# Performance work log

Hardware: AMD Instinct MI355X
Metric: run time of the kernel (lower is better)

The kernel has to match this reference:

```python
import jax, jax.numpy as jnp
import numpy as np

N = 50000   # nodes
E = 800000  # edges (avg degree 16)
F = 128     # n_input
H = 8       # n_heads
C = 16      # n_hidden (per-head out channels)
D = H * C   # 128


def setup_inputs() -> dict:
    key = jax.random.key(0)
    ks = jax.random.split(key, 12)
    s = lambda k, shape: (jax.random.normal(k, shape, dtype=jnp.float32) * 0.05)
    return {
        'x': jax.random.normal(ks[0], (N, F), dtype=jnp.float32),
        'edge_index': jax.random.randint(ks[1], (2, E), 0, N, dtype=jnp.int32),
        # GATv2Conv params (PyG defaults: share_weights=False, bias=True, neg_slope=0.2, self-loops)
        'W_l': s(ks[2], (F, D)),
        'b_l': jnp.zeros((D,), jnp.float32),
        'W_r': s(ks[3], (F, D)),
        'b_r': jnp.zeros((D,), jnp.float32),
        'att': s(ks[4], (H, C)),
        'conv_bias': jnp.zeros((D,), jnp.float32),
        # BatchNorm1d affine params
        'bn_gamma': jnp.ones((D,), jnp.float32),
        'bn_beta': jnp.zeros((D,), jnp.float32),
        # encoder output Linear
        'lin_W': s(ks[5], (D, D)),
        'lin_b': jnp.zeros((D,), jnp.float32),
        # EdgeDecoder scalars a, b (init 1.0)
        'a_edge': jnp.ones((1,), jnp.float32),
        'b_edge': jnp.ones((1,), jnp.float32),
        # LinearDecoder
        'dec2_W': s(ks[6], (D, F)),
        'dec2_b': jnp.zeros((F,), jnp.float32),
    }


def reference(x, edge_index, W_l, b_l, W_r, b_r, att, conv_bias,
              bn_gamma, bn_beta, lin_W, lin_b, a_edge, b_edge, dec2_W, dec2_b):
    n = x.shape[0]
    # GATv2Conv adds self-loops by default
    loop = jnp.arange(n, dtype=edge_index.dtype)
    src = jnp.concatenate([edge_index[0], loop])  # source j (messages come from)
    dst = jnp.concatenate([edge_index[1], loop])  # target i (softmax segments)
    xl = (x @ W_l + b_l).reshape(n, H, C)  # source transform
    xr = (x @ W_r + b_r).reshape(n, H, C)  # target transform
    # attention logits: a^T LeakyReLU(xl_j + xr_i), per head
    e = jax.nn.leaky_relu(xl[src] + xr[dst], negative_slope=0.2)  # [Et,H,C]
    logits = jnp.einsum('ehc,hc->eh', e, att)                     # [Et,H]
    # segment softmax over incoming edges of each target node
    m = jax.ops.segment_max(logits, dst, num_segments=n)
    ex = jnp.exp(logits - m[dst])
    denom = jax.ops.segment_sum(ex, dst, num_segments=n)
    alpha = ex / (denom[dst] + 1e-16)                             # [Et,H]
    # scatter-sum weighted source features, concat heads, add bias
    out = jax.ops.segment_sum(alpha[:, :, None] * xl[src], dst, num_segments=n)
    Hfeat = jax.nn.relu(out.reshape(n, D) + conv_bias)
    # BatchNorm1d, training-mode batch statistics (biased var), eps=1e-5
    mean = Hfeat.mean(axis=0)
    var = Hfeat.var(axis=0)
    Hn = (Hfeat - mean) / jnp.sqrt(var + 1e-5) * bn_gamma + bn_beta
    z = Hn @ lin_W + lin_b                                        # [N,D]
    # EdgeDecoder: gather + squared-diff + reduce over original edges
    dist = jnp.sum((z[edge_index[0]] - z[edge_index[1]]) ** 2, axis=1)  # [E]
    dist = jax.nn.relu(a_edge) * dist + b_edge
    value1 = jax.nn.sigmoid(-dist)                                # [E]
    # LinearDecoder
    value2 = z @ dec2_W + dec2_b                                  # [N,F]
    return (z, value1, value2)
```

## Files before the change

### kernel.cpp

```cpp
#include <hip/hip_runtime.h>

#define DD 128
#define HH 8
#define NBCOPY 32

typedef float f32x4 __attribute__((ext_vector_type(4)));
typedef short s16x8 __attribute__((ext_vector_type(8)));

__device__ __forceinline__ ushort f2b(float f) {
  unsigned u = __float_as_uint(f);
  unsigned r = u + 0x7fffu + ((u >> 16) & 1u);
  return (ushort)(r >> 16);
}
__device__ __forceinline__ float b2f(ushort b) {
  return __uint_as_float(((unsigned)b) << 16);
}
__device__ __forceinline__ void atomAddF(float* p, float v) {
#if defined(__HIP_DEVICE_COMPILE__)
  unsafeAtomicAdd(p, v);
#else
  atomicAdd(p, v);
#endif
}
__device__ __forceinline__ float lrelu(float v) { return fmaxf(v, 0.2f * v); }

__device__ __forceinline__ float sumC(const float* __restrict__ b8, int idx) {
  float s = 0.f;
#pragma unroll
  for (int c = 0; c < NBCOPY; c++) s += b8[(c << 8) + idx];
  return s;
}

__device__ __forceinline__ void packW_idx(int i, int& k, int& n) {
  int j = i & 7, l = (i >> 3) & 63, tile = i >> 9;
  int q = tile >> 3, c = tile & 7;
  k = q * 32 + ((l >> 4) << 3) + j;
  n = c * 16 + (l & 15);
}

__global__ __launch_bounds__(256) void k_prep(const float* __restrict__ x,
    ushort* __restrict__ xb, int total4, const float* __restrict__ Wl,
    const float* __restrict__ Wr, ushort* __restrict__ WlP,
    ushort* __restrict__ WrP, const int* __restrict__ ei,
    int* __restrict__ deg, int E, int convB, int packB) {
  int b = blockIdx.x;
  if (b < convB) {
    int i = b * 256 + threadIdx.x;
    if (i < total4) {
      float4 v = ((const float4*)x)[i];
      ushort4 o;
      o.x = f2b(v.x); o.y = f2b(v.y); o.z = f2b(v.z); o.w = f2b(v.w);
      ((ushort4*)xb)[i] = o;
    }
  } else if (b < convB + packB) {
    int t = (b - convB) * 256 + threadIdx.x;
    int side = t >> 14;
    int i = t & 16383;
    int k, n;
    packW_idx(i, k, n);
    if (side) WrP[i] = f2b(Wr[k * DD + n]);
    else      WlP[i] = f2b(Wl[k * DD + n]);
  } else {
    int e = (b - convB - packB) * 256 + threadIdx.x;
    if (e < E) atomicAdd(&deg[ei[E + e]], 1);
  }
}

__global__ __launch_bounds__(256) void k_part(const int* __restrict__ deg,
    int* __restrict__ rowstart, int* __restrict__ bsum, int N) {
  __shared__ int sc[256];
  int t = threadIdx.x;
  int i = blockIdx.x * 256 + t;
  int v = (i < N) ? deg[i] : 0;
  sc[t] = v;
  __syncthreads();
  for (int off = 1; off < 256; off <<= 1) {
    int u = (t >= off) ? sc[t - off] : 0;
    __syncthreads();
    sc[t] += u;
    __syncthreads();
  }
  if (i < N) rowstart[i] = sc[t] - v;
  if (t == 255) bsum[blockIdx.x] = sc[255];
}

__global__ __launch_bounds__(1024) void k_mid(const int* __restrict__ bsum,
    int* __restrict__ boff, int* __restrict__ rowstartN, int B) {
  __shared__ int sc[1024];
  int t = threadIdx.x;
  int v = (t < B) ? bsum[t] : 0;
  sc[t] = v;
  __syncthreads();
  for (int off = 1; off < 1024; off <<= 1) {
    int u = (t >= off) ? sc[t - off] : 0;
    __syncthreads();
    sc[t] += u;
    __syncthreads();
  }
  if (t < B) boff[t] = sc[t] - v;
  if (t == 1023) *rowstartN = sc[1023];
}

__global__ __launch_bounds__(256) void k_apply(int* __restrict__ rowstart,
    int* __restrict__ cursor, const int* __restrict__ boff, int N) {
  int i = blockIdx.x * 256 + threadIdx.x;
  if (i < N) {
    int r = rowstart[i] + boff[blockIdx.x];
    rowstart[i] = r;
    cursor[i] = r;
  }
}

__global__ __launch_bounds__(256) void k_fill(const int* __restrict__ ei,
    int* __restrict__ cursor, int* __restrict__ csr_src, int E) {
  int e = blockIdx.x * 256 + threadIdx.x;
  if (e < E) {
    int d = ei[E + e];
    int pos = atomicAdd(&cursor[d], 1);
    csr_src[pos] = ei[e];
  }
}

__global__ __launch_bounds__(256) void k_mm_lr(const ushort* __restrict__ xb,
    const ushort* __restrict__ WlP, const ushort* __restrict__ WrP,
    const float* __restrict__ bl, const float* __restrict__ br,
    ushort* __restrict__ xlb, ushort* __restrict__ xrb, int N) {
  __shared__ ushort sW[2][16384];
  {
    const uint4* a = (const uint4*)WlP;
    const uint4* b = (const uint4*)WrP;
    uint4* da = (uint4*)sW[0];
    uint4* db = (uint4*)sW[1];
    for (int i = threadIdx.x; i < 2048; i += 256) { da[i] = a[i]; db[i] = b[i]; }
  }
  __syncthreads();
  int lane = threadIdx.x & 63;
  int wv = threadIdx.x >> 6;
  int rbase = blockIdx.x * 64 + wv * 16;
  int arow = rbase + (lane & 15);
  if (arow >= N) arow = 0;
  const ushort* ap = xb + (size_t)arow * DD + ((lane >> 4) << 3);
  s16x8 afr[4];
#pragma unroll
  for (int q = 0; q < 4; q++) afr[q] = *(const s16x8*)(ap + q * 32);
  f32x4 accL[8] = {}, accR[8] = {};
#pragma unroll
  for (int q = 0; q < 4; q++) {
#pragma unroll
    for (int c = 0; c < 8; c++) {
      s16x8 bL = *(const s16x8*)(sW[0] + ((q * 8 + c) * 64 + lane) * 8);
      accL[c] = __builtin_amdgcn_mfma_f32_16x16x32_bf16(afr[q], bL, accL[c], 0, 0, 0);
      s16x8 bR = *(const s16x8*)(sW[1] + ((q * 8 + c) * 64 + lane) * 8);
      accR[c] = __builtin_amdgcn_mfma_f32_16x16x32_bf16(afr[q], bR, accR[c], 0, 0, 0);
    }
  }
  int r0 = rbase + ((lane >> 4) << 2);
  int colb = lane & 15;
#pragma unroll
  for (int c = 0; c < 8; c++) {
    int col = c * 16 + colb;
    float vbl = bl[col], vbr = br[col];
#pragma unroll
    for (int r = 0; r < 4; r++) {
      int row = r0 + r;
      if (row < N) {
        xlb[(size_t)row * DD + col] = f2b(accL[c][r] + vbl);
        xrb[(size_t)row * DD + col] = f2b(accR[c][r] + vbr);
      }
    }
  }
}

__global__ __launch_bounds__(256) void k_mm_z(const ushort* __restrict__ hfb,
    const ushort* __restrict__ W1P, const ushort* __restrict__ W2P,
    const float* __restrict__ b1p, const float* __restrict__ b2pp,
    float* __restrict__ z, ushort* __restrict__ zb, float* __restrict__ v2,
    int N) {
  __shared__ ushort sW[2][16384];
  {
    const uint4* a = (const uint4*)W1P;
    const uint4* b = (const uint4*)W2P;
    uint4* da = (uint4*)sW[0];
    uint4* db = (uint4*)sW[1];
    for (int i = threadIdx.x; i < 2048; i += 256) { da[i] = a[i]; db[i] = b[i]; }
  }
  __syncthreads();
  int lane = threadIdx.x & 63;
  int wv = threadIdx.x >> 6;
  int rbase = blockIdx.x * 64 + wv * 16;
  int arow = rbase + (lane & 15);
  if (arow >= N) arow = 0;
  const ushort* ap = hfb + (size_t)arow * DD + ((lane >> 4) << 3);
  s16x8 afr[4];
#pragma unroll
  for (int q = 0; q < 4; q++) afr[q] = *(const s16x8*)(ap + q * 32);
  f32x4 acc1[8] = {}, acc2[8] = {};
#pragma unroll
  for (int q = 0; q < 4; q++) {
#pragma unroll
    for (int c = 0; c < 8; c++) {
      s16x8 b1 = *(const s16x8*)(sW[0] + ((q * 8 + c) * 64 + lane) * 8);
      acc1[c] = __builtin_amdgcn_mfma_f32_16x16x32_bf16(afr[q], b1, acc1[c], 0, 0, 0);
      s16x8 b2 = *(const s16x8*)(sW[1] + ((q * 8 + c) * 64 + lane) * 8);
      acc2[c] = __builtin_amdgcn_mfma_f32_16x16x32_bf16(afr[q], b2, acc2[c], 0, 0, 0);
    }
  }
  int r0 = rbase + ((lane >> 4) << 2);
  int colb = lane & 15;
#pragma unroll
  for (int c = 0; c < 8; c++) {
    int col = c * 16 + colb;
    float vb1 = b1p[col], vb2 = b2pp[col];
#pragma unroll
    for (int r = 0; r < 4; r++) {
      int row = r0 + r;
      if (row < N) {
        float zv = acc1[c][r] + vb1;
        z[(size_t)row * DD + col] = zv;
        zb[(size_t)row * DD + col] = f2b(zv);
        v2[(size_t)row * DD + col] = acc2[c][r] + vb2;
      }
    }
  }
}

__global__ __launch_bounds__(256) void k_agg(const ushort* __restrict__ xlb,
    const ushort* __restrict__ xrb, const int* __restrict__ rowstart,
    const int* __restrict__ csr_src, const float* __restrict__ att,
    const float* __restrict__ cb, ushort* __restrict__ hfb,
    float* __restrict__ bnsumC, int N) {
  int lane = threadIdx.x & 63;
  int wv = threadIdx.x >> 6;
  int d = (blockIdx.x * 256 + threadIdx.x) >> 6;
  bool active = d < N;
  int dc = active ? d : 0;
  float2 a = ((const float2*)att)[lane];
  float2 c = ((const float2*)cb)[lane];
  float vx = 0.f, vy = 0.f;
  {
    ushort2 rv = ((const ushort2*)(xrb + (size_t)dc * DD))[lane];
    float2 r = {b2f(rv.x), b2f(rv.y)};
    ushort2 gv = ((const ushort2*)(xlb + (size_t)dc * DD))[lane];
    float2 g0 = {b2f(gv.x), b2f(gv.y)};
    float t0 = lrelu(g0.x + r.x) * a.x + lrelu(g0.y + r.y) * a.y;
#pragma unroll
    for (int o = 4; o; o >>= 1) t0 += __shfl_xor(t0, o);
    float m0 = t0;
    float den0 = 1.f, den1 = 0.f, den2 = 0.f, den3 = 0.f;
    float2 acc0 = g0, acc1 = {0.f, 0.f}, acc2 = {0.f, 0.f}, acc3 = {0.f, 0.f};
    int i0 = rowstart[dc], i1 = active ? rowstart[dc + 1] : i0;
    int i = i0;
    for (; i + 4 <= i1; i += 4) {
      int s0 = csr_src[i], s1 = csr_src[i + 1];
      int s2 = csr_src[i + 2], s3 = csr_src[i + 3];
      ushort2 va = ((const ushort2*)(xlb + (size_t)s0 * DD))[lane];
      ushort2 vb = ((const ushort2*)(xlb + (size_t)s1 * DD))[lane];
      ushort2 vc = ((const ushort2*)(xlb + (size_t)s2 * DD))[lane];
      ushort2 vd = ((const ushort2*)(xlb + (size_t)s3 * DD))[lane];
      float2 ga = {b2f(va.x), b2f(va.y)};
      float2 gb = {b2f(vb.x), b2f(vb.y)};
      float2 gc = {b2f(vc.x), b2f(vc.y)};
      float2 gd = {b2f(vd.x), b2f(vd.y)};
      float ta = lrelu(ga.x + r.x) * a.x + lrelu(ga.y + r.y) * a.y;
      float tb = lrelu(gb.x + r.x) * a.x + lrelu(gb.y + r.y) * a.y;
      float tc = lrelu(gc.x + r.x) * a.x + lrelu(gc.y + r.y) * a.y;
      float td = lrelu(gd.x + r.x) * a.x + lrelu(gd.y + r.y) * a.y;
#pragma unroll
      for (int o = 4; o; o >>= 1) {
        ta += __shfl_xor(ta, o);
        tb += __shfl_xor(tb, o);
        tc += __shfl_xor(tc, o);
        td += __shfl_xor(td, o);
      }
      float ea = __expf(fminf(ta - m0, 60.f));
      float eb = __expf(fminf(tb - m0, 60.f));
      float ec = __expf(fminf(tc - m0, 60.f));
      float ed = __expf(fminf(td - m0, 60.f));
      den0 += ea; acc0.x += ea * ga.x; acc0.y += ea * ga.y;
      den1 += eb; acc1.x += eb * gb.x; acc1.y += eb * gb.y;
      den2 += ec; acc2.x += ec * gc.x; acc2.y += ec * gc.y;
      den3 += ed; acc3.x += ed * gd.x; acc3.y += ed * gd.y;
    }
    for (; i < i1; i++) {
      int s = csr_src[i];
      ushort2 va = ((const ushort2*)(xlb + (size_t)s * DD))[lane];
      float2 ga = {b2f(va.x), b2f(va.y)};
      float ta = lrelu(ga.x + r.x) * a.x + lrelu(ga.y + r.y) * a.y;
#pragma unroll
      for (int o = 4; o; o >>= 1) ta += __shfl_xor(ta, o);
      float ea = __expf(fminf(ta - m0, 60.f));
      den0 += ea;
      acc0.x += ea * ga.x;
      acc0.y += ea * ga.y;
    }
    float den = ((den0 + den1) + (den2 + den3)) + 1e-16f;
    float ax = (acc0.x + acc1.x) + (acc2.x + acc3.x);
    float ay = (acc0.y + acc1.y) + (acc2.y + acc3.y);
    float inv = 1.f / den;
    if (active) {
      vx = fmaxf(fmaf(ax, inv, c.x), 0.f);
      vy = fmaxf(fmaf(ay, inv, c.y), 0.f);
      ushort2 o2;
      o2.x = f2b(vx);
      o2.y = f2b(vy);
      ((ushort2*)(hfb + (size_t)dc * DD))[lane] = o2;
    }
  }
  __shared__ float4 red[4][64];
  red[wv][lane] = make_float4(vx, vx * vx, vy, vy * vy);
  __syncthreads();
  if (wv == 0) {
    float4 p0 = red[0][lane], p1 = red[1][lane];
    float4 p2 = red[2][lane], p3 = red[3][lane];
    float* bs = bnsumC + ((blockIdx.x & (NBCOPY - 1)) << 8);
    atomAddF(&bs[2 * lane],           (p0.x + p1.x) + (p2.x + p3.x));
    atomAddF(&bs[2 * lane + 1],       (p0.z + p1.z) + (p2.z + p3.z));
    atomAddF(&bs[DD + 2 * lane],      (p0.y + p1.y) + (p2.y + p3.y));
    atomAddF(&bs[DD + 2 * lane + 1],  (p0.w + p1.w) + (p2.w + p3.w));
  }
}

__global__ __launch_bounds__(256) void k_fold(const float* __restrict__ bnsumC,
    const float* __restrict__ gamma, const float* __restrict__ beta,
    const float* __restrict__ linW, const float* __restrict__ linb,
    const float* __restrict__ dec2W, const float* __restrict__ dec2b,
    float* __restrict__ b1p, float* __restrict__ b2pp,
    ushort* __restrict__ W1P, ushort* __restrict__ W2P, int N) {
  int b = blockIdx.x;
  float invN = 1.f / (float)N;
  if (b == 0) {
    int t = threadIdx.x;
    __shared__ float sshift[DD], sb1[DD];
    if (t < DD) {
      float mean = sumC(bnsumC, t) * invN;
      float var = sumC(bnsumC, DD + t) * invN - mean * mean;
      float sc = gamma[t] / sqrtf(var + 1e-5f);
      sshift[t] = beta[t] - mean * sc;
    }
    __syncthreads();
    if (t < DD) {
      float b1 = linb[t];
#pragma unroll 8
      for (int k = 0; k < DD; k++) b1 += sshift[k] * linW[k * DD + t];
      b1p[t] = b1;
      sb1[t] = b1;
    }
    __syncthreads();
    if (t < DD) {
      float b2v = dec2b[t];
#pragma unroll 8
      for (int k = 0; k < DD; k++) b2v += sb1[k] * dec2W[k * DD + t];
      b2pp[t] = b2v;
    }
  } else if (b <= 64) {
    int i = (b - 1) * 256 + threadIdx.x;
    int k, n;
    packW_idx(i, k, n);
    float mean = sumC(bnsumC, k) * invN;
    float var = sumC(bnsumC, DD + k) * invN - mean * mean;
    float sc = gamma[k] / sqrtf(var + 1e-5f);
    float s = 0.f;
#pragma unroll 8
    for (int kk = 0; kk < DD; kk++) s += linW[k * DD + kk] * dec2W[kk * DD + n];
    W2P[i] = f2b(sc * s);
  } else {
    int i = (b - 65) * 256 + threadIdx.x;
    int k, n;
    packW_idx(i, k, n);
    float mean = sumC(bnsumC, k) * invN;
    float var = sumC(bnsumC, DD + k) * invN - mean * mean;
    float sc = gamma[k] / sqrtf(var + 1e-5f);
    W1P[i] = f2b(sc * linW[k * DD + n]);
  }
}

__global__ __launch_bounds__(256) void k_edge(const ushort* __restrict__ zb,
    const int* __restrict__ ei, const float* __restrict__ ae,
    const float* __restrict__ be, float* __restrict__ v1, int E) {
  int lane = threadIdx.x & 63;
  int sub = lane >> 4;
  int cl = lane & 15;
  int wid = (blockIdx.x * 256 + threadIdx.x) >> 6;
  int nw = (gridDim.x * 256) >> 6;
  int nq = (E + 3) >> 2;
  float a = fmaxf(ae[0], 0.f), b = be[0];
  for (int q = wid; q < nq; q += nw) {
    int e = q * 4 + sub;
    bool ok = e < E;
    int ec = ok ? e : 0;
    int s = ei[ec], d = ei[E + ec];
    uint4 zs = *(const uint4*)(zb + (size_t)s * DD + cl * 8);
    uint4 zd = *(const uint4*)(zb + (size_t)d * DD + cl * 8);
    float v = 0.f;
    float dl, dh;
    dl = __uint_as_float(zs.x << 16) - __uint_as_float(zd.x << 16);
    dh = __uint_as_float(zs.x & 0xffff0000u) - __uint_as_float(zd.x & 0xffff0000u);
    v += dl * dl + dh * dh;
    dl = __uint_as_float(zs.y << 16) - __uint_as_float(zd.y << 16);
    dh = __uint_as_float(zs.y & 0xffff0000u) - __uint_as_float(zd.y & 0xffff0000u);
    v += dl * dl + dh * dh;
    dl = __uint_as_float(zs.z << 16) - __uint_as_float(zd.z << 16);
    dh = __uint_as_float(zs.z & 0xffff0000u) - __uint_as_float(zd.z & 0xffff0000u);
    v += dl * dl + dh * dh;
    dl = __uint_as_float(zs.w << 16) - __uint_as_float(zd.w << 16);
    dh = __uint_as_float(zs.w & 0xffff0000u) - __uint_as_float(zd.w & 0xffff0000u);
    v += dl * dl + dh * dh;
#pragma unroll
    for (int o = 8; o; o >>= 1) v += __shfl_xor(v, o);
    if (cl == 0 && ok) v1[e] = 1.f / (1.f + __expf(fmaf(a, v, b)));
  }
}

extern "C" void kernel_launch(void* const* d_in, const int* in_sizes, int n_in,
                              void* d_out, int out_size, void* d_ws, size_t ws_size,
                              hipStream_t stream) {
  const float* x = (const float*)d_in[0];
  const int* ei = (const int*)d_in[1];
  const float* Wl = (const float*)d_in[2];
  const float* bl = (const float*)d_in[3];
  const float* Wr = (const float*)d_in[4];
  const float* br = (const float*)d_in[5];
  const float* att = (const float*)d_in[6];
  const float* cb = (const float*)d_in[7];
  const float* gamma = (const float*)d_in[8];
  const float* beta = (const float*)d_in[9];
  const float* linW = (const float*)d_in[10];
  const float* linb = (const float*)d_in[11];
  const float* ae = (const float*)d_in[12];
  const float* be = (const float*)d_in[13];
  const float* dec2W = (const float*)d_in[14];
  const float* dec2b = (const float*)d_in[15];

  int N = in_sizes[0] / DD;
  int E = in_sizes[1] / 2;
  size_t ND = (size_t)N * DD;
  int B = (N + 255) / 256;

  char* wsb = (char*)d_ws;
  size_t o = 0;
  auto alloc = [&](size_t bytes) {
    void* p = wsb + o;
    o += (bytes + 15) & ~(size_t)15;
    return p;
  };
  ushort* xb  = (ushort*)alloc(ND * 2);
  ushort* xlb = (ushort*)alloc(ND * 2);
  ushort* xrb = (ushort*)alloc(ND * 2);
  ushort* hfb = (ushort*)alloc(ND * 2);
  ushort* zbb = (ushort*)alloc(ND * 2);
  ushort* WlP = (ushort*)alloc(DD * DD * 2);
  ushort* WrP = (ushort*)alloc(DD * DD * 2);
  ushort* W1P = (ushort*)alloc(DD * DD * 2);
  ushort* W2P = (ushort*)alloc(DD * DD * 2);
  float* b1p   = (float*)alloc(DD * 4);
  float* b2pp  = (float*)alloc(DD * 4);
  int* deg       = (int*)alloc((size_t)(N + 1) * 4);
  float* bnsumC  = (float*)alloc(NBCOPY * 2 * DD * 4);
  size_t clearBytes = (char*)(bnsumC + NBCOPY * 2 * DD) - (char*)deg;
  int* rowstart = (int*)alloc((size_t)(N + 1) * 4);
  int* cursor   = (int*)alloc((size_t)N * 4);
  int* bsum     = (int*)alloc((size_t)B * 4);
  int* boff     = (int*)alloc((size_t)B * 4);
  int* csr_src  = (int*)alloc((size_t)E * 4);

  float* z = (float*)d_out;
  float* v1 = z + ND;
  float* v2 = v1 + E;

  hipMemsetAsync(deg, 0, clearBytes, stream);

  int total4 = (int)(ND / 4);
  int convB = (total4 + 255) / 256;
  int packB = 128;
  int degB = (E + 255) / 256;
  k_prep<<<convB + packB + degB, 256, 0, stream>>>(x, xb, total4, Wl, Wr, WlP,
                                                   WrP, ei, deg, E, convB, packB);
  k_part<<<B, 256, 0, stream>>>(deg, rowstart, bsum, N);
  k_mid<<<1, 1024, 0, stream>>>(bsum, boff, rowstart + N, B);
  k_apply<<<B, 256, 0, stream>>>(rowstart, cursor, boff, N);
  k_fill<<<(E + 255) / 256, 256, 0, stream>>>(ei, cursor, csr_src, E);
  k_mm_lr<<<(N + 63) / 64, 256, 0, stream>>>(xb, WlP, WrP, bl, br, xlb, xrb, N);
  k_agg<<<(N + 3) / 4, 256, 0, stream>>>(xlb, xrb, rowstart, csr_src, att, cb,
                                         hfb, bnsumC, N);
  k_fold<<<129, 256, 0, stream>>>(bnsumC, gamma, beta, linW, linb, dec2W,
                                  dec2b, b1p, b2pp, W1P, W2P, N);
  k_mm_z<<<(N + 63) / 64, 256, 0, stream>>>(hfb, W1P, W2P, b1p, b2pp, z, zbb,
                                            v2, N);
  k_edge<<<2048, 256, 0, stream>>>(zbb, ei, ae, be, v1, E);
}
```

Before: 267.4 us.

## Fuse CSR fill into x-transform GEMM, split z GEMM, overlap v2 with edge decoder

The CSR fill runs in the same launch as the xl/xr GEMM, and the v2 decoder GEMM runs in the same launch as the edge-distance kernel, using block-index ranges. This lets independent work overlap and removes kernel launches. The GEMMs now read packed weights straight from global memory instead of staging them in LDS. The deg and cursor counters are padded with a stride of 16 ints so that atomics on neighbouring nodes land on separate cache lines. The costs are a larger memset, more global reads of the weights, and heterogeneous blocks inside one grid.

```diff
diff --git a/kernel.cpp b/kernel.cpp
--- a/kernel.cpp
+++ b/kernel.cpp
@@ -3,6 +3,7 @@
 #define DD 128
 #define HH 8
 #define NBCOPY 32
+#define PADS 4
 
 typedef float f32x4 __attribute__((ext_vector_type(4)));
 typedef short s16x8 __attribute__((ext_vector_type(8)));
@@ -62,7 +63,7 @@
     else      WlP[i] = f2b(Wl[k * DD + n]);
   } else {
     int e = (b - convB - packB) * 256 + threadIdx.x;
-    if (e < E) atomicAdd(&deg[ei[E + e]], 1);
+    if (e < E) atomicAdd(&deg[ei[E + e] << PADS], 1);
   }
 }
 
@@ -71,7 +72,7 @@
   __shared__ int sc[256];
   int t = threadIdx.x;
   int i = blockIdx.x * 256 + t;
-  int v = (i < N) ? deg[i] : 0;
+  int v = (i < N) ? deg[i << PADS] : 0;
   sc[t] = v;
   __syncthreads();
   for (int off = 1; off < 256; off <<= 1) {
@@ -107,33 +108,25 @@
   if (i < N) {
     int r = rowstart[i] + boff[blockIdx.x];
     rowstart[i] = r;
-    cursor[i] = r;
-  }
-}
-
-__global__ __launch_bounds__(256) void k_fill(const int* __restrict__ ei,
-    int* __restrict__ cursor, int* __restrict__ csr_src, int E) {
-  int e = blockIdx.x * 256 + threadIdx.x;
-  if (e < E) {
-    int d = ei[E + e];
-    int pos = atomicAdd(&cursor[d], 1);
-    csr_src[pos] = ei[e];
-  }
-}
-
-__global__ __launch_bounds__(256) void k_mm_lr(const ushort* __restrict__ xb,
+    cursor[i << PADS] = r;
+  }
+}
+
+__global__ __launch_bounds__(256) void k_lrfill(const ushort* __restrict__ xb,
     const ushort* __restrict__ WlP, const ushort* __restrict__ WrP,
     const float* __restrict__ bl, const float* __restrict__ br,
-    ushort* __restrict__ xlb, ushort* __restrict__ xrb, int N) {
-  __shared__ ushort sW[2][16384];
-  {
-    const uint4* a = (const uint4*)WlP;
-    const uint4* b = (const uint4*)WrP;
-    uint4* da = (uint4*)sW[0];
-    uint4* db = (uint4*)sW[1];
-    for (int i = threadIdx.x; i < 2048; i += 256) { da[i] = a[i]; db[i] = b[i]; }
-  }
-  __syncthreads();
+    ushort* __restrict__ xlb, ushort* __restrict__ xrb, int N, int mmB,
+    const int* __restrict__ ei, int* __restrict__ cursor,
+    int* __restrict__ csr_src, int E) {
+  if ((int)blockIdx.x >= mmB) {
+    int e = ((int)blockIdx.x - mmB) * 256 + threadIdx.x;
+    if (e < E) {
+      int d = ei[E + e];
+      int pos = atomicAdd(&cursor[d << PADS], 1);
+      csr_src[pos] = ei[e];
+    }
+    return;
+  }
   int lane = threadIdx.x & 63;
   int wv = threadIdx.x >> 6;
   int rbase = blockIdx.x * 64 + wv * 16;
@@ -143,15 +136,17 @@
   s16x8 afr[4];
 #pragma unroll
   for (int q = 0; q < 4; q++) afr[q] = *(const s16x8*)(ap + q * 32);
+  const s16x8* BL = (const s16x8*)WlP;
+  const s16x8* BR = (const s16x8*)WrP;
   f32x4 accL[8] = {}, accR[8] = {};
 #pragma unroll
   for (int q = 0; q < 4; q++) {
 #pragma unroll
     for (int c = 0; c < 8; c++) {
-      s16x8 bL = *(const s16x8*)(sW[0] + ((q * 8 + c) * 64 + lane) * 8);
-      accL[c] = __builtin_amdgcn_mfma_f32_16x16x32_bf16(afr[q], bL, accL[c], 0, 0, 0);
-      s16x8 bR = *(const s16x8*)(sW[1] + ((q * 8 + c) * 64 + lane) * 8);
-      accR[c] = __builtin_amdgcn_mfma_f32_16x16x32_bf16(afr[q], bR, accR[c], 0, 0, 0);
+      accL[c] = __builtin_amdgcn_mfma_f32_16x16x32_bf16(
+          afr[q], BL[(q * 8 + c) * 64 + lane], accL[c], 0, 0, 0);
+      accR[c] = __builtin_amdgcn_mfma_f32_16x16x32_bf16(
+          afr[q], BR[(q * 8 + c) * 64 + lane], accR[c], 0, 0, 0);
     }
   }
   int r0 = rbase + ((lane >> 4) << 2);
@@ -166,59 +161,6 @@
       if (row < N) {
         xlb[(size_t)row * DD + col] = f2b(accL[c][r] + vbl);
         xrb[(size_t)row * DD + col] = f2b(accR[c][r] + vbr);
-      }
-    }
-  }
-}
-
-__global__ __launch_bounds__(256) void k_mm_z(const ushort* __restrict__ hfb,
-    const ushort* __restrict__ W1P, const ushort* __restrict__ W2P,
-    const float* __restrict__ b1p, const float* __restrict__ b2pp,
-    float* __restrict__ z, ushort* __restrict__ zb, float* __restrict__ v2,
-    int N) {
-  __shared__ ushort sW[2][16384];
-  {
-    const uint4* a = (const uint4*)W1P;
-    const uint4* b = (const uint4*)W2P;
-    uint4* da = (uint4*)sW[0];
-    uint4* db = (uint4*)sW[1];
-    for (int i = threadIdx.x; i < 2048; i += 256) { da[i] = a[i]; db[i] = b[i]; }
-  }
-  __syncthreads();
-  int lane = threadIdx.x & 63;
-  int wv = threadIdx.x >> 6;
-  int rbase = blockIdx.x * 64 + wv * 16;
-  int arow = rbase + (lane & 15);
-  if (arow >= N) arow = 0;
-  const ushort* ap = hfb + (size_t)arow * DD + ((lane >> 4) << 3);
-  s16x8 afr[4];
-#pragma unroll
-  for (int q = 0; q < 4; q++) afr[q] = *(const s16x8*)(ap + q * 32);
-  f32x4 acc1[8] = {}, acc2[8] = {};
-#pragma unroll
-  for (int q = 0; q < 4; q++) {
-#pragma unroll
-    for (int c = 0; c < 8; c++) {
-      s16x8 b1 = *(const s16x8*)(sW[0] + ((q * 8 + c) * 64 + lane) * 8);
-      acc1[c] = __builtin_amdgcn_mfma_f32_16x16x32_bf16(afr[q], b1, acc1[c], 0, 0, 0);
-      s16x8 b2 = *(const s16x8*)(sW[1] + ((q * 8 + c) * 64 + lane) * 8);
-      acc2[c] = __builtin_amdgcn_mfma_f32_16x16x32_bf16(afr[q], b2, acc2[c], 0, 0, 0);
-    }
-  }
-  int r0 = rbase + ((lane >> 4) << 2);
-  int colb = lane & 15;
-#pragma unroll
-  for (int c = 0; c < 8; c++) {
-    int col = c * 16 + colb;
-    float vb1 = b1p[col], vb2 = b2pp[col];
-#pragma unroll
-    for (int r = 0; r < 4; r++) {
-      int row = r0 + r;
-      if (row < N) {
-        float zv = acc1[c][r] + vb1;
-        z[(size_t)row * DD + col] = zv;
-        zb[(size_t)row * DD + col] = f2b(zv);
-        v2[(size_t)row * DD + col] = acc2[c][r] + vb2;
       }
     }
   }
@@ -374,14 +316,91 @@
   }
 }
 
-__global__ __launch_bounds__(256) void k_edge(const ushort* __restrict__ zb,
-    const int* __restrict__ ei, const float* __restrict__ ae,
-    const float* __restrict__ be, float* __restrict__ v1, int E) {
+__global__ __launch_bounds__(256) void k_mmz1(const ushort* __restrict__ hfb,
+    const ushort* __restrict__ W1P, const float* __restrict__ b1p,
+    float* __restrict__ z, ushort* __restrict__ zb, int N) {
+  int lane = threadIdx.x & 63;
+  int wv = threadIdx.x >> 6;
+  int rbase = blockIdx.x * 64 + wv * 16;
+  int arow = rbase + (lane & 15);
+  if (arow >= N) arow = 0;
+  const ushort* ap = hfb + (size_t)arow * DD + ((lane >> 4) << 3);
+  s16x8 afr[4];
+#pragma unroll
+  for (int q = 0; q < 4; q++) afr[q] = *(const s16x8*)(ap + q * 32);
+  const s16x8* B1 = (const s16x8*)W1P;
+  f32x4 acc1[8] = {};
+#pragma unroll
+  for (int q = 0; q < 4; q++) {
+#pragma unroll
+    for (int c = 0; c < 8; c++) {
+      acc1[c] = __builtin_amdgcn_mfma_f32_16x16x32_bf16(
+          afr[q], B1[(q * 8 + c) * 64 + lane], acc1[c], 0, 0, 0);
+    }
+  }
+  int r0 = rbase + ((lane >> 4) << 2);
+  int colb = lane & 15;
+#pragma unroll
+  for (int c = 0; c < 8; c++) {
+    int col = c * 16 + colb;
+    float vb1 = b1p[col];
+#pragma unroll
+    for (int r = 0; r < 4; r++) {
+      int row = r0 + r;
+      if (row < N) {
+        float zv = acc1[c][r] + vb1;
+        z[(size_t)row * DD + col] = zv;
+        zb[(size_t)row * DD + col] = f2b(zv);
+      }
+    }
+  }
+}
+
+__global__ __launch_bounds__(256) void k_v2edge(const ushort* __restrict__ hfb,
+    const ushort* __restrict__ W2P, const float* __restrict__ b2pp,
+    float* __restrict__ v2, int N, int v2B,
+    const ushort* __restrict__ zb, const int* __restrict__ ei,
+    const float* __restrict__ ae, const float* __restrict__ be,
+    float* __restrict__ v1, int E, int edgeB) {
+  if ((int)blockIdx.x < v2B) {
+    int lane = threadIdx.x & 63;
+    int wv = threadIdx.x >> 6;
+    int rbase = blockIdx.x * 64 + wv * 16;
+    int arow = rbase + (lane & 15);
+    if (arow >= N) arow = 0;
+    const ushort* ap = hfb + (size_t)arow * DD + ((lane >> 4) << 3);
+    s16x8 afr[4];
+#pragma unroll
+    for (int q = 0; q < 4; q++) afr[q] = *(const s16x8*)(ap + q * 32);
+    const s16x8* B2 = (const s16x8*)W2P;
+    f32x4 acc2[8] = {};
+#pragma unroll
+    for (int q = 0; q < 4; q++) {
+#pragma unroll
+      for (int c = 0; c < 8; c++) {
+        acc2[c] = __builtin_amdgcn_mfma_f32_16x16x32_bf16(
+            afr[q], B2[(q * 8 + c) * 64 + lane], acc2[c], 0, 0, 0);
+      }
+    }
+    int r0 = rbase + ((lane >> 4) << 2);
+    int colb = lane & 15;
+#pragma unroll
+    for (int c = 0; c < 8; c++) {
+      int col = c * 16 + colb;
+      float vb2 = b2pp[col];
+#pragma unroll
+      for (int r = 0; r < 4; r++) {
+        int row = r0 + r;
+        if (row < N) v2[(size_t)row * DD + col] = acc2[c][r] + vb2;
+      }
+    }
+    return;
+  }
   int lane = threadIdx.x & 63;
   int sub = lane >> 4;
   int cl = lane & 15;
-  int wid = (blockIdx.x * 256 + threadIdx.x) >> 6;
-  int nw = (gridDim.x * 256) >> 6;
+  int wid = (((int)blockIdx.x - v2B) * 256 + threadIdx.x) >> 6;
+  int nw = (edgeB * 256) >> 6;
   int nq = (E + 3) >> 2;
   float a = fmaxf(ae[0], 0.f), b = be[0];
   for (int q = wid; q < nq; q += nw) {
@@ -454,11 +473,11 @@
   ushort* W2P = (ushort*)alloc(DD * DD * 2);
   float* b1p   = (float*)alloc(DD * 4);
   float* b2pp  = (float*)alloc(DD * 4);
-  int* deg       = (int*)alloc((size_t)(N + 1) * 4);
+  int* deg       = (int*)alloc(((size_t)N << PADS) * 4 + 64);
   float* bnsumC  = (float*)alloc(NBCOPY * 2 * DD * 4);
   size_t clearBytes = (char*)(bnsumC + NBCOPY * 2 * DD) - (char*)deg;
   int* rowstart = (int*)alloc((size_t)(N + 1) * 4);
-  int* cursor   = (int*)alloc((size_t)N * 4);
+  int* cursor   = (int*)alloc(((size_t)N << PADS) * 4 + 64);
   int* bsum     = (int*)alloc((size_t)B * 4);
   int* boff     = (int*)alloc((size_t)B * 4);
   int* csr_src  = (int*)alloc((size_t)E * 4);
@@ -478,13 +497,17 @@
   k_part<<<B, 256, 0, stream>>>(deg, rowstart, bsum, N);
   k_mid<<<1, 1024, 0, stream>>>(bsum, boff, rowstart + N, B);
   k_apply<<<B, 256, 0, stream>>>(rowstart, cursor, boff, N);
-  k_fill<<<(E + 255) / 256, 256, 0, stream>>>(ei, cursor, csr_src, E);
-  k_mm_lr<<<(N + 63) / 64, 256, 0, stream>>>(xb, WlP, WrP, bl, br, xlb, xrb, N);
+  int mmB = (N + 63) / 64;
+  int fillB = (E + 255) / 256;
+  k_lrfill<<<mmB + fillB, 256, 0, stream>>>(xb, WlP, WrP, bl, br, xlb, xrb, N,
+                                            mmB, ei, cursor, csr_src, E);
   k_agg<<<(N + 3) / 4, 256, 0, stream>>>(xlb, xrb, rowstart, csr_src, att, cb,
                                          hfb, bnsumC, N);
   k_fold<<<129, 256, 0, stream>>>(bnsumC, gamma, beta, linW, linb, dec2W,
                                   dec2b, b1p, b2pp, W1P, W2P, N);
-  k_mm_z<<<(N + 63) / 64, 256, 0, stream>>>(hfb, W1P, W2P, b1p, b2pp, z, zbb,
-                                            v2, N);
-  k_edge<<<2048, 256, 0, stream>>>(zbb, ei, ae, be, v1, E);
-}
+  k_mmz1<<<(N + 63) / 64, 256, 0, stream>>>(hfb, W1P, b1p, z, zbb, N);
+  int v2B = (N + 63) / 64;
+  int edgeB = 2048;
+  k_v2edge<<<v2B + edgeB, 256, 0, stream>>>(hfb, W2P, b2pp, v2, N, v2B, zbb,
+                                            ei, ae, be, v1, E, edgeB);
+}
```

New measurement: 241.9 us. 9.5% less time.
